# Performance work log

Measured on AMD Instinct MI355X. Metric: run time of the kernel, lower is better.

## Reference

```python
import jax, jax.numpy as jnp
import numpy as np

B, GRID, CIN, COUT, TDIM, NMODES = 32, 128, 32, 32, 256, 32
M = NMODES // 2 + 1  # kept modes per axis = 17
FFT_NORM = 'forward'


def setup_inputs() -> dict:
    key = jax.random.key(0)
    ks = jax.random.split(key, 10)
    w_std = float(np.sqrt(1.0 / (2.0 * CIN)))          # normal_initializer(in_co_dim)
    k_std = float(np.sqrt(1.0 / TDIM))                 # ~lecun_normal for Dense kernels
    wshape = (M, M, CIN, COUT)
    return {
        'x': jax.random.normal(ks[0], (B, GRID, GRID, CIN), jnp.float32),
        't_emb': jax.random.normal(ks[1], (B, TDIM), jnp.float32),
        'w1_real': w_std * jax.random.normal(ks[2], wshape, jnp.float32),
        'w1_imag': w_std * jax.random.normal(ks[3], wshape, jnp.float32),
        'w2_real': w_std * jax.random.normal(ks[4], wshape, jnp.float32),
        'w2_imag': w_std * jax.random.normal(ks[5], wshape, jnp.float32),
        'k1_real': k_std * jax.random.normal(ks[6], (TDIM, M), jnp.float32),
        'k1_imag': k_std * jax.random.normal(ks[7], (TDIM, M), jnp.float32),
        'k2_real': k_std * jax.random.normal(ks[8], (TDIM, M), jnp.float32),
        'k2_imag': k_std * jax.random.normal(ks[9], (TDIM, M), jnp.float32),
    }


def reference(x, t_emb, w1_real, w1_imag, w2_real, w2_imag,
              k1_real, k1_imag, k2_real, k2_imag):
    b, n = x.shape[0], x.shape[1]
    # rFFT2 over spatial axes: (b, n, n//2+1, cin) complex
    x_ft = jnp.fft.rfft2(x, axes=(1, 2), norm=FFT_NORM)

    w1 = w1_real + 1j * w1_imag  # (M, M, cin, cout)
    w2 = w2_real + 1j * w2_imag
    # Time modulation: Dense(no bias) -> complex per-mode scale t[b, i].
    # The original builds diag(t) and einsums it into the weights; that equals a
    # simple broadcast scale over the first mode axis, fused here.
    t1 = (t_emb @ k1_real) + 1j * (t_emb @ k1_imag)  # (b, M)
    t2 = (t_emb @ k2_real) + 1j * (t_emb @ k2_imag)

    # Mode-truncated complex channel contraction, scaled by t along axis i.
    xf1 = jnp.einsum('bijc,ijco->bijo', x_ft[:, :M, :M, :], w1) * t1[:, :, None, None]
    xf2 = jnp.einsum('bijc,ijco->bijo', x_ft[:, -M:, :M, :], w2) * t2[:, :, None, None]

    out_ft = jnp.zeros((b, n, n // 2 + 1, COUT), dtype=jnp.complex64)
    out_ft = out_ft.at[:, :M, :M, :].set(xf1)
    out_ft = out_ft.at[:, -M:, :M, :].set(xf2)

    return jnp.fft.irfft2(out_ft, s=(n, n), axes=(1, 2), norm=FFT_NORM)
```

## Files before the change

### kernel.cpp

```cpp
#include <hip/hip_runtime.h>
#include <stdint.h>


#define TWO_PI_OVER_128 0.04908738521234052f

__global__ __launch_bounds__(128) void k_tproj(
    const float* __restrict__ temb, const float* __restrict__ k1r, const float* __restrict__ k1i,
    const float* __restrict__ k2r, const float* __restrict__ k2i, float* __restrict__ tbuf)
{
    int b = blockIdx.x, tid = threadIdx.x;
    __shared__ float ts[256];
    for (int d = tid; d < 256; d += 128) ts[d] = temb[b * 256 + d];
    __syncthreads();
    if (tid < 68) {
        int which = (tid >= 34) ? 1 : 0;
        int rem = tid - which * 34;
        int i = rem >> 1, part = rem & 1;
        const float* kp = which ? (part ? k2i : k2r) : (part ? k1i : k1r);
        float a0 = 0.f, a1 = 0.f, a2 = 0.f, a3 = 0.f;
        for (int d = 0; d < 256; d += 4) {
            a0 = fmaf(ts[d],     kp[(d)     * 17 + i], a0);
            a1 = fmaf(ts[d + 1], kp[(d + 1) * 17 + i], a1);
            a2 = fmaf(ts[d + 2], kp[(d + 2) * 17 + i], a2);
            a3 = fmaf(ts[d + 3], kp[(d + 3) * 17 + i], a3);
        }
        tbuf[((which * 32 + b) * 17 + i) * 2 + part] = (a0 + a1) + (a2 + a3);
    }
}

__global__ __launch_bounds__(64) void k_fwd_y(const float* __restrict__ x, float2* __restrict__ T1)
{
    int blk = blockIdx.x;
    int b = blk >> 7, xr = blk & 127;
    __shared__ float xs[128 * 32];
    __shared__ float2 cst[128];
    int tid = threadIdx.x;
    {
        float s0, c0; sincosf(TWO_PI_OVER_128 * (float)tid, &s0, &c0);
        cst[tid] = make_float2(c0, -s0);
        float s1, c1; sincosf(TWO_PI_OVER_128 * (float)(tid + 64), &s1, &c1);
        cst[tid + 64] = make_float2(c1, -s1);
    }
    const float4* xv = (const float4*)(x + ((size_t)blk << 12));
    float4* xs4 = (float4*)xs;
#pragma unroll
    for (int i = 0; i < 16; ++i) xs4[tid + (i << 6)] = xv[tid + (i << 6)];
    __syncthreads();
    for (int i = tid; i < 2016; i += 64) {
        int y = (i >> 5) + 1, c = i & 31;
        float a = xs[(y << 5) + c], q = xs[((128 - y) << 5) + c];
        xs[(y << 5) + c] = a + q;
        xs[((128 - y) << 5) + c] = a - q;
    }
    __syncthreads();
    int jg = tid >> 3, cg = tid & 7, c0 = cg << 2;
    float re[2][4] = {{0,0,0,0},{0,0,0,0}}, im[2][4] = {{0,0,0,0},{0,0,0,0}};
    int j0 = jg, j1 = jg + 8;
    int idx0 = 0, idx1 = 0;
    for (int y = 1; y <= 63; ++y) {
        idx0 = (idx0 + j0) & 127;
        idx1 = (idx1 + j1) & 127;
        float2 w0 = cst[idx0], w1 = cst[idx1];
        float4 s = *(const float4*)&xs[(y << 5) + c0];
        float4 d = *(const float4*)&xs[((128 - y) << 5) + c0];
        re[0][0] = fmaf(s.x, w0.x, re[0][0]);
        re[0][1] = fmaf(s.y, w0.x, re[0][1]);
        re[0][2] = fmaf(s.z, w0.x, re[0][2]);
        re[0][3] = fmaf(s.w, w0.x, re[0][3]);
        im[0][0] = fmaf(d.x, w0.y, im[0][0]);
        im[0][1] = fmaf(d.y, w0.y, im[0][1]);
        im[0][2] = fmaf(d.z, w0.y, im[0][2]);
        im[0][3] = fmaf(d.w, w0.y, im[0][3]);
        re[1][0] = fmaf(s.x, w1.x, re[1][0]);
        re[1][1] = fmaf(s.y, w1.x, re[1][1]);
        re[1][2] = fmaf(s.z, w1.x, re[1][2]);
        re[1][3] = fmaf(s.w, w1.x, re[1][3]);
        im[1][0] = fmaf(d.x, w1.y, im[1][0]);
        im[1][1] = fmaf(d.y, w1.y, im[1][1]);
        im[1][2] = fmaf(d.z, w1.y, im[1][2]);
        im[1][3] = fmaf(d.w, w1.y, im[1][3]);
    }
    const float s_ = 1.f / 16384.f;
    float x0[4], x64[4];
    *(float4*)x0  = *(const float4*)&xs[c0];
    *(float4*)x64 = *(const float4*)&xs[(64 << 5) + c0];
#pragma unroll
    for (int t = 0; t < 2; ++t) {
        int j = jg + t * 8;
        float sg = (j & 1) ? -1.f : 1.f;
        float2* p = T1 + (((size_t)(b * 17 + j) * 128 + xr) << 5) + c0;
        float4 v0 = make_float4((re[t][0] + x0[0] + sg * x64[0]) * s_, im[t][0] * s_,
                                (re[t][1] + x0[1] + sg * x64[1]) * s_, im[t][1] * s_);
        float4 v1 = make_float4((re[t][2] + x0[2] + sg * x64[2]) * s_, im[t][2] * s_,
                                (re[t][3] + x0[3] + sg * x64[3]) * s_, im[t][3] * s_);
        ((float4*)p)[0] = v0; ((float4*)p)[1] = v1;
    }
    if (jg == 0) {
        float re2[4] = {0,0,0,0}, im2[4] = {0,0,0,0};
        int idx2 = 0;
        for (int y = 1; y <= 63; ++y) {
            idx2 = (idx2 + 16) & 127;
            float2 w = cst[idx2];
            float4 s = *(const float4*)&xs[(y << 5) + c0];
            float4 d = *(const float4*)&xs[((128 - y) << 5) + c0];
            re2[0] = fmaf(s.x, w.x, re2[0]); re2[1] = fmaf(s.y, w.x, re2[1]);
            re2[2] = fmaf(s.z, w.x, re2[2]); re2[3] = fmaf(s.w, w.x, re2[3]);
            im2[0] = fmaf(d.x, w.y, im2[0]); im2[1] = fmaf(d.y, w.y, im2[1]);
            im2[2] = fmaf(d.z, w.y, im2[2]); im2[3] = fmaf(d.w, w.y, im2[3]);
        }
        float2* p = T1 + (((size_t)(b * 17 + 16) * 128 + xr) << 5) + c0;
        float4 v0 = make_float4((re2[0] + x0[0] + x64[0]) * s_, im2[0] * s_,
                                (re2[1] + x0[1] + x64[1]) * s_, im2[1] * s_);
        float4 v1 = make_float4((re2[2] + x0[2] + x64[2]) * s_, im2[2] * s_,
                                (re2[3] + x0[3] + x64[3]) * s_, im2[3] * s_);
        ((float4*)p)[0] = v0; ((float4*)p)[1] = v1;
    }
}

__global__ __launch_bounds__(512) void k_mid_fused(
    const float2* __restrict__ T1, const float* __restrict__ w1r, const float* __restrict__ w1i,
    const float* __restrict__ w2r, const float* __restrict__ w2i,
    const float* __restrict__ tbuf, float2* __restrict__ U)
{
    int blk = blockIdx.x;
    int b = blk / 17, j = blk - b * 17;
    __shared__ float4 Ts4[2048];
    __shared__ float2 Xf[34 * 32];
    __shared__ float2 cst[128];
    int tid = threadIdx.x;
    const float4* s4 = (const float4*)(T1 + (size_t)blk * 4096);
    for (int i = tid; i < 2048; i += 512) Ts4[i] = s4[i];
    if (tid < 128) {
        float s, c; sincosf(TWO_PI_OVER_128 * (float)tid, &s, &c);
        cst[tid] = make_float2(c, s);
    }
    __syncthreads();
    for (int i = tid; i < 1008; i += 512) {
        int xx = (i >> 4) + 1, cp = i & 15;
        float4 a = Ts4[(xx << 4) + cp], q = Ts4[((128 - xx) << 4) + cp];
        Ts4[(xx << 4) + cp] = make_float4(a.x + q.x, a.y + q.y, a.z + q.z, a.w + q.w);
        Ts4[((128 - xx) << 4) + cp] = make_float4(a.x - q.x, a.y - q.y, a.z - q.z, a.w - q.w);
    }
    __syncthreads();
    if (tid < 288) {
        int cp = tid & 15, u = tid >> 4;
        float4 t0 = Ts4[cp], t64 = Ts4[(64 << 4) + cp];
        if (u < 16) {
            int f = u + 1;
            int idx = 0;
            float P0=0,Q0=0,R0=0,T0=0,P1=0,Q1=0,R1=0,T1a=0;
            for (int xx = 1; xx <= 63; ++xx) {
                idx = (idx + f) & 127;
                float2 w = cst[idx];
                float4 S = Ts4[(xx << 4) + cp];
                float4 D = Ts4[((128 - xx) << 4) + cp];
                P0 = fmaf(S.x, w.x, P0); Q0 = fmaf(D.y, w.y, Q0);
                R0 = fmaf(S.y, w.x, R0); T0 = fmaf(D.x, w.y, T0);
                P1 = fmaf(S.z, w.x, P1); Q1 = fmaf(D.w, w.y, Q1);
                R1 = fmaf(S.w, w.x, R1); T1a = fmaf(D.z, w.y, T1a);
            }
            float sg = (f & 1) ? -1.f : 1.f;
            float b0r = t0.x + sg * t64.x, b0i = t0.y + sg * t64.y;
            float b1r = t0.z + sg * t64.z, b1i = t0.w + sg * t64.w;
            int ia = f, ib = 34 - f;
            Xf[ia * 32 + cp*2]   = make_float2(P0 + Q0 + b0r, R0 - T0 + b0i);
            Xf[ia * 32 + cp*2+1] = make_float2(P1 + Q1 + b1r, R1 - T1a + b1i);
            Xf[ib * 32 + cp*2]   = make_float2(P0 - Q0 + b0r, R0 + T0 + b0i);
            Xf[ib * 32 + cp*2+1] = make_float2(P1 - Q1 + b1r, R1 + T1a + b1i);
        } else if (u == 16) {
            float A0=0,B0=0,A1=0,B1=0;
            for (int xx = 1; xx <= 63; ++xx) {
                float4 S = Ts4[(xx << 4) + cp];
                A0 += S.x; B0 += S.y; A1 += S.z; B1 += S.w;
            }
            Xf[cp*2]   = make_float2(A0 + t0.x + t64.x, B0 + t0.y + t64.y);
            Xf[cp*2+1] = make_float2(A1 + t0.z + t64.z, B1 + t0.w + t64.w);
        } else {
            int idx = 0;
            float p0=0,q0=0,r0=0,s0=0,p1=0,q1=0,r1=0,s1=0;
            for (int xx = 1; xx <= 63; ++xx) {
                idx = (idx + 111) & 127;
                float2 w = cst[idx];
                float4 S = Ts4[(xx << 4) + cp];
                float4 D = Ts4[((128 - xx) << 4) + cp];
                p0 = fmaf(S.x, w.x, p0); q0 = fmaf(D.y, w.y, q0);
                r0 = fmaf(S.y, w.x, r0); s0 = fmaf(D.x, w.y, s0);
                p1 = fmaf(S.z, w.x, p1); q1 = fmaf(D.w, w.y, q1);
                r1 = fmaf(S.w, w.x, r1); s1 = fmaf(D.z, w.y, s1);
            }
            float c0r = t0.x - t64.x, c0i = t0.y - t64.y;
            float c1r = t0.z - t64.z, c1i = t0.w - t64.w;
            Xf[17*32 + cp*2]   = make_float2(p0 + q0 + c0r, r0 - s0 + c0i);
            Xf[17*32 + cp*2+1] = make_float2(p1 + q1 + c1r, r1 - s1 + c1i);
        }
    }
    __syncthreads();
    float2* Ys = (float2*)Ts4;
    if (tid < 272) {
        int oq = tid & 7, ii = tid >> 3;
        int o0 = oq << 2;
        int irow = (ii < 17) ? ii : ii - 17;
        const float* wr = ((ii < 17) ? w1r : w2r) + ((irow * 17 + j) << 10) + o0;
        const float* wi = ((ii < 17) ? w1i : w2i) + ((irow * 17 + j) << 10) + o0;
        float ar0=0,ai0=0,ar1=0,ai1=0,ar2=0,ai2=0,ar3=0,ai3=0;
#pragma unroll 4
        for (int c = 0; c < 32; ++c) {
            float2 xv = Xf[ii * 32 + c];
            float4 wre = *(const float4*)(wr + (c << 5));
            float4 wim = *(const float4*)(wi + (c << 5));
            ar0 = fmaf(xv.x, wre.x, ar0); ar0 = fmaf(-xv.y, wim.x, ar0);
            ai0 = fmaf(xv.x, wim.x, ai0); ai0 = fmaf( xv.y, wre.x, ai0);
            ar1 = fmaf(xv.x, wre.y, ar1); ar1 = fmaf(-xv.y, wim.y, ar1);
            ai1 = fmaf(xv.x, wim.y, ai1); ai1 = fmaf( xv.y, wre.y, ai1);
            ar2 = fmaf(xv.x, wre.z, ar2); ar2 = fmaf(-xv.y, wim.z, ar2);
            ai2 = fmaf(xv.x, wim.z, ai2); ai2 = fmaf( xv.y, wre.z, ai2);
            ar3 = fmaf(xv.x, wre.w, ar3); ar3 = fmaf(-xv.y, wim.w, ar3);
            ai3 = fmaf(xv.x, wim.w, ai3); ai3 = fmaf( xv.y, wre.w, ai3);
        }
        int which = (ii >= 17) ? 1 : 0;
        const float* tp = tbuf + ((which * 32 + b) * 17 + irow) * 2;
        float tr = tp[0], ti = tp[1];
        float2* yp = Ys + ii * 32 + o0;
        float4 y01 = make_float4(ar0 * tr - ai0 * ti, ar0 * ti + ai0 * tr,
                                 ar1 * tr - ai1 * ti, ar1 * ti + ai1 * tr);
        float4 y23 = make_float4(ar2 * tr - ai2 * ti, ar2 * ti + ai2 * tr,
                                 ar3 * tr - ai3 * ti, ar3 * ti + ai3 * tr);
        ((float4*)yp)[0] = y01;
        ((float4*)yp)[1] = y23;
    }
    __syncthreads();
    {
        int o = tid & 31, g = tid >> 5;
        float yr[34], yi[34];
#pragma unroll
        for (int i = 0; i < 34; ++i) { float2 v = Ys[i * 32 + o]; yr[i] = v.x; yi[i] = v.y; }
        float2* Ub = U + ((size_t)b * 128 * 17 + j) * 32 + o;
        if (g == 0) {
            float sr = 0.f, si = 0.f;
#pragma unroll
            for (int i = 0; i < 34; ++i) { sr += yr[i]; si += yi[i]; }
            Ub[0] = make_float2(sr, si);
        }
        for (int k = 0; k < 4; ++k) {
            int x = 1 + g + (k << 4);
            if (x == 64) {
                float sr = 0.f, si = 0.f;
#pragma unroll
                for (int i = 0; i < 34; ++i) {
                    float sg2 = (i & 1) ? -1.f : 1.f;
                    sr = fmaf(sg2, yr[i], sr); si = fmaf(sg2, yi[i], si);
                }
                Ub[(size_t)64 * 544] = make_float2(sr, si);
            } else {
                float A1=0,A2=0,A3=0,A4=0;
                int idx = 0;
#pragma unroll
                for (int i = 0; i < 17; ++i) {
                    float2 w = cst[idx];
                    A1 = fmaf(yr[i], w.x, A1); A4 = fmaf(yr[i], w.y, A4);
                    A3 = fmaf(yi[i], w.x, A3); A2 = fmaf(yi[i], w.y, A2);
                    idx = (idx + x) & 127;
                }
                idx = (111 * x) & 127;
#pragma unroll
                for (int i = 17; i < 34; ++i) {
                    float2 w = cst[idx];
                    A1 = fmaf(yr[i], w.x, A1); A4 = fmaf(yr[i], w.y, A4);
                    A3 = fmaf(yi[i], w.x, A3); A2 = fmaf(yi[i], w.y, A2);
                    idx = (idx + x) & 127;
                }
                Ub[(size_t)x * 544]         = make_float2(A1 - A2, A3 + A4);
                Ub[(size_t)(128 - x) * 544] = make_float2(A1 + A2, A3 - A4);
            }
        }
    }
}

__global__ __launch_bounds__(256) void k_fwd_x_mix(
    const float2* __restrict__ T1, const float* __restrict__ w1r, const float* __restrict__ w1i,
    const float* __restrict__ w2r, const float* __restrict__ w2i,
    const float* __restrict__ tbuf, float2* __restrict__ Y)
{
    int blk = blockIdx.x;
    int b = blk / 17, j = blk - b * 17;
    __shared__ float4 Ts4[2048];
    __shared__ float2 Xf[34 * 32];
    int tid = threadIdx.x;
    const float4* s4 = (const float4*)(T1 + (size_t)blk * 4096);
    for (int i = tid; i < 2048; i += 256) Ts4[i] = s4[i];
    __syncthreads();
    {
        int cp = tid & 15, g = tid >> 4;
        int il[3] = {g, g + 16, g + 32};
        float stc[3], sts[3];
#pragma unroll
        for (int t = 0; t < 3; ++t) {
            int i = il[t];
            int f = (i < 17) ? i : i + 94;
            float a = -TWO_PI_OVER_128 * (float)(f & 127);
            sincosf(a, &sts[t], &stc[t]);
        }
        float cr[3] = {1.f, 1.f, 1.f}, ci[3] = {0.f, 0.f, 0.f};
        float r0[3] = {0,0,0}, i0[3] = {0,0,0}, r1[3] = {0,0,0}, i1[3] = {0,0,0};
        const float4* Tc = Ts4 + cp;
#pragma unroll 2
        for (int xx = 0; xx < 128; ++xx) {
            float4 tv = Tc[xx << 4];
#pragma unroll
            for (int t = 0; t < 3; ++t) {
                r0[t] += tv.x * cr[t] - tv.y * ci[t];
                i0[t] += tv.x * ci[t] + tv.y * cr[t];
                r1[t] += tv.z * cr[t] - tv.w * ci[t];
                i1[t] += tv.z * ci[t] + tv.w * cr[t];
                float nr = cr[t] * stc[t] - ci[t] * sts[t];
                ci[t] = fmaf(cr[t], sts[t], ci[t] * stc[t]);
                cr[t] = nr;
            }
        }
#pragma unroll
        for (int t = 0; t < 3; ++t) {
            int i = il[t];
            if (i < 34) {
                Xf[i * 32 + cp * 2]     = make_float2(r0[t], i0[t]);
                Xf[i * 32 + cp * 2 + 1] = make_float2(r1[t], i1[t]);
            }
        }
    }
    __syncthreads();
    {
        int o = tid & 31, gi = tid >> 5;
#pragma unroll
        for (int t = 0; t < 5; ++t) {
            int ii = gi + (t << 3);
            if (ii < 34) {
                int irow = (ii < 17) ? ii : ii - 17;
                const float* wr = ((ii < 17) ? w1r : w2r) + ((irow * 17 + j) << 10) + o;
                const float* wi = ((ii < 17) ? w1i : w2i) + ((irow * 17 + j) << 10) + o;
                float ar = 0.f, ai = 0.f;
#pragma unroll 8
                for (int cc2 = 0; cc2 < 32; ++cc2) {
                    float2 xv = Xf[ii * 32 + cc2];
                    float wre = wr[cc2 << 5];
                    float wim = wi[cc2 << 5];
                    ar += xv.x * wre - xv.y * wim;
                    ai += xv.x * wim + xv.y * wre;
                }
                int which = (ii >= 17) ? 1 : 0;
                const float* tp = tbuf + ((which * 32 + b) * 17 + irow) * 2;
                float tr = tp[0], ti = tp[1];
                Y[(size_t)blk * (34 * 32) + ii * 32 + o] =
                    make_float2(ar * tr - ai * ti, ar * ti + ai * tr);
            }
        }
    }
}

__global__ __launch_bounds__(256) void k_inv_x(const float2* __restrict__ Y, float2* __restrict__ U)
{
    int blk = blockIdx.x;
    int b = blk / 17, j = blk - b * 17;
    __shared__ float2 Ys[34 * 32];
    __shared__ float ct[128], st[128];
    int tid = threadIdx.x;
    if (tid < 128) {
        float a = TWO_PI_OVER_128 * (float)tid;
        sincosf(a, &st[tid], &ct[tid]);
    }
    const float2* src = Y + (size_t)blk * (34 * 32);
    for (int i = tid; i < 34 * 32; i += 256) Ys[i] = src[i];
    __syncthreads();
    int o = tid & 31, g = tid >> 5;
    float yr[34], yi[34];
#pragma unroll
    for (int i = 0; i < 34; ++i) { float2 v = Ys[i * 32 + o]; yr[i] = v.x; yi[i] = v.y; }
    for (int xi = 0; xi < 16; ++xi) {
        int xr = (xi << 3) + g;
        float cx = ct[xr], sx = st[xr];
        float cr = 1.f, ci = 0.f, re = 0.f, im = 0.f;
#pragma unroll
        for (int i = 0; i < 17; ++i) {
            re += yr[i] * cr - yi[i] * ci;
            im += yr[i] * ci + yi[i] * cr;
            float nr = cr * cx - ci * sx;
            ci = fmaf(cr, sx, ci * cx);
            cr = nr;
        }
        int k2 = (111 * xr) & 127;
        cr = ct[k2]; ci = st[k2];
#pragma unroll
        for (int i = 17; i < 34; ++i) {
            re += yr[i] * cr - yi[i] * ci;
            im += yr[i] * ci + yi[i] * cr;
            float nr = cr * cx - ci * sx;
            ci = fmaf(cr, sx, ci * cx);
            cr = nr;
        }
        U[(((size_t)(b * 128 + xr)) * 17 + j) * 32 + o] = make_float2(re, im);
    }
}

__global__ __launch_bounds__(128) void k_inv_y(const float2* __restrict__ U, float* __restrict__ out)
{
    int blk = blockIdx.x;
    __shared__ float2 Us[17 * 32];
    __shared__ float2 cst[128];
    int tid = threadIdx.x;
    {
        float s, c; sincosf(TWO_PI_OVER_128 * (float)tid, &s, &c);
        cst[tid] = make_float2(c, s);
    }
    const float4* src4 = (const float4*)(U + (size_t)blk * 544);
    float4* Us4 = (float4*)Us;
    for (int i = tid; i < 272; i += 128) Us4[i] = src4[i];
    __syncthreads();
    int cg = tid & 15, yg = tid >> 4, c0 = cg << 1;
    float base0, base1;
    {
        float4 v = *(const float4*)&Us[c0];
        base0 = v.x; base1 = v.z;
    }
    float urr[16][2], uii[16][2];
#pragma unroll
    for (int jj = 1; jj <= 16; ++jj) {
        float4 v = *(const float4*)&Us[jj * 32 + c0];
        urr[jj-1][0] = 2.f * v.x; uii[jj-1][0] = 2.f * v.y;
        urr[jj-1][1] = 2.f * v.z; uii[jj-1][1] = 2.f * v.w;
    }
    float* op = out + ((size_t)blk << 12);
    for (int k = 0; k < 9; ++k) {
        int y = yg + (k << 3);
        if (y > 64) break;
        float A0 = 0.f, A1 = 0.f, B0 = 0.f, B1 = 0.f;
        int idx = y;
#pragma unroll
        for (int jj = 0; jj < 16; ++jj) {
            float2 w = cst[idx];
            A0 = fmaf(urr[jj][0], w.x, A0);
            B0 = fmaf(uii[jj][0], w.y, B0);
            A1 = fmaf(urr[jj][1], w.x, A1);
            B1 = fmaf(uii[jj][1], w.y, B1);
            idx = (idx + y) & 127;
        }
        *(float2*)&op[(y << 5) + c0] = make_float2(base0 + A0 - B0, base1 + A1 - B1);
        if (y > 0 && y < 64)
            *(float2*)&op[((128 - y) << 5) + c0] = make_float2(base0 + A0 + B0, base1 + A1 + B1);
    }
}

extern "C" void kernel_launch(void* const* d_in, const int* in_sizes, int n_in,
                              void* d_out, int out_size, void* d_ws, size_t ws_size,
                              hipStream_t stream)
{
    const float* x    = (const float*)d_in[0];
    const float* temb = (const float*)d_in[1];
    const float* w1r  = (const float*)d_in[2];
    const float* w1i  = (const float*)d_in[3];
    const float* w2r  = (const float*)d_in[4];
    const float* w2i  = (const float*)d_in[5];
    const float* k1r  = (const float*)d_in[6];
    const float* k1i  = (const float*)d_in[7];
    const float* k2r  = (const float*)d_in[8];
    const float* k2i  = (const float*)d_in[9];
    float* out = (float*)d_out;

    char* ws = (char*)d_ws;
    const size_t T1_BYTES = 17825792;
    const size_t NEED_FUSED = 2 * T1_BYTES + 8704;

    if (ws_size >= NEED_FUSED) {
        float2* T1 = (float2*)ws;
        float2* U  = (float2*)(ws + T1_BYTES);
        float*  tb = (float*)(ws + 2 * T1_BYTES);
        k_tproj    <<<32,   128, 0, stream>>>(temb, k1r, k1i, k2r, k2i, tb);
        k_fwd_y    <<<4096, 64,  0, stream>>>(x, T1);
        k_mid_fused<<<544,  512, 0, stream>>>(T1, w1r, w1i, w2r, w2i, tb, U);
        k_inv_y    <<<4096, 128, 0, stream>>>(U, out);
    } else {
        float2* T1 = (float2*)ws;
        float2* Yb = (float2*)(ws + T1_BYTES);
        float*  tb = (float*)(ws + T1_BYTES + 4734976);
        float2* U  = T1;
        k_tproj    <<<32,   128, 0, stream>>>(temb, k1r, k1i, k2r, k2i, tb);
        k_fwd_y    <<<4096, 64,  0, stream>>>(x, T1);
        k_fwd_x_mix<<<544,  256, 0, stream>>>(T1, w1r, w1i, w2r, w2i, tb, Yb);
        k_inv_x    <<<544,  256, 0, stream>>>(Yb, U);
        k_inv_y    <<<4096, 128, 0, stream>>>(U, out);
    }
}
```

Baseline: 198.2 us.

## Exploit even/odd twiddle symmetry in inverse DFTs and parallelize Nyquist column

The forward Nyquist-mode (j=16) sum, which a single thread group used to compute alone, is now split across all eight jg groups and combined with cross-lane shuffle reductions. The inverse x and y DFT stages split their accumulators into even and odd terms, so one pass over the inputs produces four outputs (x, 128-x, 64-x, 64+x) through the half-period sign flip. This halves the twiddle loop iterations and removes load imbalance. The Xf shared array row stride is also padded to 34 to reduce LDS bank conflicts. The cost is more accumulator registers and more complex index bookkeeping.

```diff
diff --git a/kernel.cpp b/kernel.cpp
--- a/kernel.cpp
+++ b/kernel.cpp
@@ -95,28 +95,38 @@
                                 (re[t][3] + x0[3] + sg * x64[3]) * s_, im[t][3] * s_);
         ((float4*)p)[0] = v0; ((float4*)p)[1] = v1;
     }
-    if (jg == 0) {
+    {
         float re2[4] = {0,0,0,0}, im2[4] = {0,0,0,0};
-        int idx2 = 0;
-        for (int y = 1; y <= 63; ++y) {
-            idx2 = (idx2 + 16) & 127;
-            float2 w = cst[idx2];
+        float2 w16 = cst[(16 * (jg + 1)) & 127];
+        for (int y = jg + 1; y <= 63; y += 8) {
             float4 s = *(const float4*)&xs[(y << 5) + c0];
             float4 d = *(const float4*)&xs[((128 - y) << 5) + c0];
-            re2[0] = fmaf(s.x, w.x, re2[0]); re2[1] = fmaf(s.y, w.x, re2[1]);
-            re2[2] = fmaf(s.z, w.x, re2[2]); re2[3] = fmaf(s.w, w.x, re2[3]);
-            im2[0] = fmaf(d.x, w.y, im2[0]); im2[1] = fmaf(d.y, w.y, im2[1]);
-            im2[2] = fmaf(d.z, w.y, im2[2]); im2[3] = fmaf(d.w, w.y, im2[3]);
-        }
-        float2* p = T1 + (((size_t)(b * 17 + 16) * 128 + xr) << 5) + c0;
-        float4 v0 = make_float4((re2[0] + x0[0] + x64[0]) * s_, im2[0] * s_,
-                                (re2[1] + x0[1] + x64[1]) * s_, im2[1] * s_);
-        float4 v1 = make_float4((re2[2] + x0[2] + x64[2]) * s_, im2[2] * s_,
-                                (re2[3] + x0[3] + x64[3]) * s_, im2[3] * s_);
-        ((float4*)p)[0] = v0; ((float4*)p)[1] = v1;
-    }
-}
-
+            re2[0] = fmaf(s.x, w16.x, re2[0]); re2[1] = fmaf(s.y, w16.x, re2[1]);
+            re2[2] = fmaf(s.z, w16.x, re2[2]); re2[3] = fmaf(s.w, w16.x, re2[3]);
+            im2[0] = fmaf(d.x, w16.y, im2[0]); im2[1] = fmaf(d.y, w16.y, im2[1]);
+            im2[2] = fmaf(d.z, w16.y, im2[2]); im2[3] = fmaf(d.w, w16.y, im2[3]);
+        }
+#pragma unroll
+        for (int t = 0; t < 4; ++t) {
+            re2[t] += __shfl_xor(re2[t], 8);
+            re2[t] += __shfl_xor(re2[t], 16);
+            re2[t] += __shfl_xor(re2[t], 32);
+            im2[t] += __shfl_xor(im2[t], 8);
+            im2[t] += __shfl_xor(im2[t], 16);
+            im2[t] += __shfl_xor(im2[t], 32);
+        }
+        if (jg == 0) {
+            float2* p = T1 + (((size_t)(b * 17 + 16) * 128 + xr) << 5) + c0;
+            float4 v0 = make_float4((re2[0] + x0[0] + x64[0]) * s_, im2[0] * s_,
+                                    (re2[1] + x0[1] + x64[1]) * s_, im2[1] * s_);
+            float4 v1 = make_float4((re2[2] + x0[2] + x64[2]) * s_, im2[2] * s_,
+                                    (re2[3] + x0[3] + x64[3]) * s_, im2[3] * s_);
+            ((float4*)p)[0] = v0; ((float4*)p)[1] = v1;
+        }
+    }
+}
+
+#define XFS 34
 __global__ __launch_bounds__(512) void k_mid_fused(
     const float2* __restrict__ T1, const float* __restrict__ w1r, const float* __restrict__ w1i,
     const float* __restrict__ w2r, const float* __restrict__ w2i,
@@ -125,7 +135,7 @@
     int blk = blockIdx.x;
     int b = blk / 17, j = blk - b * 17;
     __shared__ float4 Ts4[2048];
-    __shared__ float2 Xf[34 * 32];
+    __shared__ float2 Xf[34 * XFS];
     __shared__ float2 cst[128];
     int tid = threadIdx.x;
     const float4* s4 = (const float4*)(T1 + (size_t)blk * 4096);
@@ -163,10 +173,10 @@
             float b0r = t0.x + sg * t64.x, b0i = t0.y + sg * t64.y;
             float b1r = t0.z + sg * t64.z, b1i = t0.w + sg * t64.w;
             int ia = f, ib = 34 - f;
-            Xf[ia * 32 + cp*2]   = make_float2(P0 + Q0 + b0r, R0 - T0 + b0i);
-            Xf[ia * 32 + cp*2+1] = make_float2(P1 + Q1 + b1r, R1 - T1a + b1i);
-            Xf[ib * 32 + cp*2]   = make_float2(P0 - Q0 + b0r, R0 + T0 + b0i);
-            Xf[ib * 32 + cp*2+1] = make_float2(P1 - Q1 + b1r, R1 + T1a + b1i);
+            Xf[ia * XFS + cp*2]   = make_float2(P0 + Q0 + b0r, R0 - T0 + b0i);
+            Xf[ia * XFS + cp*2+1] = make_float2(P1 + Q1 + b1r, R1 - T1a + b1i);
+            Xf[ib * XFS + cp*2]   = make_float2(P0 - Q0 + b0r, R0 + T0 + b0i);
+            Xf[ib * XFS + cp*2+1] = make_float2(P1 - Q1 + b1r, R1 + T1a + b1i);
         } else if (u == 16) {
             float A0=0,B0=0,A1=0,B1=0;
             for (int xx = 1; xx <= 63; ++xx) {
@@ -190,8 +200,8 @@
             }
             float c0r = t0.x - t64.x, c0i = t0.y - t64.y;
             float c1r = t0.z - t64.z, c1i = t0.w - t64.w;
-            Xf[17*32 + cp*2]   = make_float2(p0 + q0 + c0r, r0 - s0 + c0i);
-            Xf[17*32 + cp*2+1] = make_float2(p1 + q1 + c1r, r1 - s1 + c1i);
+            Xf[17*XFS + cp*2]   = make_float2(p0 + q0 + c0r, r0 - s0 + c0i);
+            Xf[17*XFS + cp*2+1] = make_float2(p1 + q1 + c1r, r1 - s1 + c1i);
         }
     }
     __syncthreads();
@@ -205,7 +215,7 @@
         float ar0=0,ai0=0,ar1=0,ai1=0,ar2=0,ai2=0,ar3=0,ai3=0;
 #pragma unroll 4
         for (int c = 0; c < 32; ++c) {
-            float2 xv = Xf[ii * 32 + c];
+            float2 xv = Xf[ii * XFS + c];
             float4 wre = *(const float4*)(wr + (c << 5));
             float4 wim = *(const float4*)(wi + (c << 5));
             ar0 = fmaf(xv.x, wre.x, ar0); ar0 = fmaf(-xv.y, wim.x, ar0);
@@ -241,37 +251,50 @@
             for (int i = 0; i < 34; ++i) { sr += yr[i]; si += yi[i]; }
             Ub[0] = make_float2(sr, si);
         }
-        for (int k = 0; k < 4; ++k) {
+        if (g == 1) {
+            float sr = 0.f, si = 0.f;
+#pragma unroll
+            for (int i = 0; i < 34; ++i) {
+                float sg2 = (i & 1) ? -1.f : 1.f;
+                sr = fmaf(sg2, yr[i], sr); si = fmaf(sg2, yi[i], si);
+            }
+            Ub[(size_t)64 * 544] = make_float2(sr, si);
+        }
+        for (int k = 0; k < 2; ++k) {
             int x = 1 + g + (k << 4);
-            if (x == 64) {
-                float sr = 0.f, si = 0.f;
-#pragma unroll
-                for (int i = 0; i < 34; ++i) {
-                    float sg2 = (i & 1) ? -1.f : 1.f;
-                    sr = fmaf(sg2, yr[i], sr); si = fmaf(sg2, yi[i], si);
+            float A1e=0,A1o=0,A2e=0,A2o=0,A3e=0,A3o=0,A4e=0,A4o=0;
+            int idx = 0;
+#pragma unroll
+            for (int i = 0; i < 17; ++i) {
+                float2 w = cst[idx];
+                if (i & 1) {
+                    A1o = fmaf(yr[i], w.x, A1o); A4o = fmaf(yr[i], w.y, A4o);
+                    A3o = fmaf(yi[i], w.x, A3o); A2o = fmaf(yi[i], w.y, A2o);
+                } else {
+                    A1e = fmaf(yr[i], w.x, A1e); A4e = fmaf(yr[i], w.y, A4e);
+                    A3e = fmaf(yi[i], w.x, A3e); A2e = fmaf(yi[i], w.y, A2e);
                 }
-                Ub[(size_t)64 * 544] = make_float2(sr, si);
-            } else {
-                float A1=0,A2=0,A3=0,A4=0;
-                int idx = 0;
-#pragma unroll
-                for (int i = 0; i < 17; ++i) {
-                    float2 w = cst[idx];
-                    A1 = fmaf(yr[i], w.x, A1); A4 = fmaf(yr[i], w.y, A4);
-                    A3 = fmaf(yi[i], w.x, A3); A2 = fmaf(yi[i], w.y, A2);
-                    idx = (idx + x) & 127;
+                idx = (idx + x) & 127;
+            }
+            idx = (111 * x) & 127;
+#pragma unroll
+            for (int i = 17; i < 34; ++i) {
+                float2 w = cst[idx];
+                if (i & 1) {
+                    A1o = fmaf(yr[i], w.x, A1o); A4o = fmaf(yr[i], w.y, A4o);
+                    A3o = fmaf(yi[i], w.x, A3o); A2o = fmaf(yi[i], w.y, A2o);
+                } else {
+                    A1e = fmaf(yr[i], w.x, A1e); A4e = fmaf(yr[i], w.y, A4e);
+                    A3e = fmaf(yi[i], w.x, A3e); A2e = fmaf(yi[i], w.y, A2e);
                 }
-                idx = (111 * x) & 127;
-#pragma unroll
-                for (int i = 17; i < 34; ++i) {
-                    float2 w = cst[idx];
-                    A1 = fmaf(yr[i], w.x, A1); A4 = fmaf(yr[i], w.y, A4);
-                    A3 = fmaf(yi[i], w.x, A3); A2 = fmaf(yi[i], w.y, A2);
-                    idx = (idx + x) & 127;
-                }
-                Ub[(size_t)x * 544]         = make_float2(A1 - A2, A3 + A4);
-                Ub[(size_t)(128 - x) * 544] = make_float2(A1 + A2, A3 - A4);
-            }
+                idx = (idx + x) & 127;
+            }
+            float A1 = A1e + A1o, A2 = A2e + A2o, A3 = A3e + A3o, A4 = A4e + A4o;
+            float E1 = A1e - A1o, E2 = A2o - A2e, E3 = A3e - A3o, E4 = A4o - A4e;
+            Ub[(size_t)x * 544]         = make_float2(A1 - A2, A3 + A4);
+            Ub[(size_t)(128 - x) * 544] = make_float2(A1 + A2, A3 - A4);
+            Ub[(size_t)(64 - x) * 544]  = make_float2(E1 - E2, E3 + E4);
+            Ub[(size_t)(64 + x) * 544]  = make_float2(E1 + E2, E3 - E4);
         }
     }
 }
@@ -427,23 +450,39 @@
         urr[jj-1][1] = 2.f * v.z; uii[jj-1][1] = 2.f * v.w;
     }
     float* op = out + ((size_t)blk << 12);
-    for (int k = 0; k < 9; ++k) {
-        int y = yg + (k << 3);
-        if (y > 64) break;
-        float A0 = 0.f, A1 = 0.f, B0 = 0.f, B1 = 0.f;
+    for (int k = 0; k < 4; ++k) {
+        int y = 1 + yg + (k << 3);
+        float Ae0=0,Ao0=0,Be0=0,Bo0=0,Ae1=0,Ao1=0,Be1=0,Bo1=0;
         int idx = y;
 #pragma unroll
         for (int jj = 0; jj < 16; ++jj) {
             float2 w = cst[idx];
-            A0 = fmaf(urr[jj][0], w.x, A0);
-            B0 = fmaf(uii[jj][0], w.y, B0);
-            A1 = fmaf(urr[jj][1], w.x, A1);
-            B1 = fmaf(uii[jj][1], w.y, B1);
+            if (jj & 1) {
+                Ae0 = fmaf(urr[jj][0], w.x, Ae0); Be0 = fmaf(uii[jj][0], w.y, Be0);
+                Ae1 = fmaf(urr[jj][1], w.x, Ae1); Be1 = fmaf(uii[jj][1], w.y, Be1);
+            } else {
+                Ao0 = fmaf(urr[jj][0], w.x, Ao0); Bo0 = fmaf(uii[jj][0], w.y, Bo0);
+                Ao1 = fmaf(urr[jj][1], w.x, Ao1); Bo1 = fmaf(uii[jj][1], w.y, Bo1);
+            }
             idx = (idx + y) & 127;
         }
-        *(float2*)&op[(y << 5) + c0] = make_float2(base0 + A0 - B0, base1 + A1 - B1);
-        if (y > 0 && y < 64)
-            *(float2*)&op[((128 - y) << 5) + c0] = make_float2(base0 + A0 + B0, base1 + A1 + B1);
+        float s0 = Ae0 + Ao0, d0 = Be0 + Bo0, e0 = Ae0 - Ao0, f0 = Be0 - Bo0;
+        float s1 = Ae1 + Ao1, d1 = Be1 + Bo1, e1 = Ae1 - Ao1, f1 = Be1 - Bo1;
+        *(float2*)&op[(y << 5) + c0]         = make_float2(base0 + s0 - d0, base1 + s1 - d1);
+        *(float2*)&op[((128 - y) << 5) + c0] = make_float2(base0 + s0 + d0, base1 + s1 + d1);
+        *(float2*)&op[((64 - y) << 5) + c0]  = make_float2(base0 + e0 + f0, base1 + e1 + f1);
+        *(float2*)&op[((64 + y) << 5) + c0]  = make_float2(base0 + e0 - f0, base1 + e1 - f1);
+    }
+    if (yg == 0) {
+        float s0 = 0.f, s1 = 0.f, a0 = 0.f, a1 = 0.f;
+#pragma unroll
+        for (int jj = 0; jj < 16; ++jj) {
+            s0 += urr[jj][0]; s1 += urr[jj][1];
+            float sg = (jj & 1) ? 1.f : -1.f;
+            a0 = fmaf(sg, urr[jj][0], a0); a1 = fmaf(sg, urr[jj][1], a1);
+        }
+        *(float2*)&op[c0]             = make_float2(base0 + s0, base1 + s1);
+        *(float2*)&op[(64 << 5) + c0] = make_float2(base0 + a0, base1 + a1);
     }
 }
 
```

Result: faster. 187.6 us (-5.3%).
